# Optimization experiments

Hardware: AMD Instinct MI355X
Metric: run time of the kernel (lower is better)

## Reference

```python
import jax, jax.numpy as jnp
import numpy as np

B = 32          # number of graphs/segments
N_PER = 1024    # nodes per graph (equal segments)
N = B * N_PER
DIM = 3
SIGMA = 0.2


def setup_inputs() -> dict:
    key = jax.random.key(0)
    k1, k2, k3, k4 = jax.random.split(key, 4)
    src_pos = jax.random.normal(k1, (N, DIM), dtype=jnp.float32)
    tgt_pos = jax.random.normal(k2, (N, DIM), dtype=jnp.float32)
    # equal-sized contiguous segments: 0,0,...,1,1,...,B-1
    src_batch = jnp.repeat(jnp.arange(B, dtype=jnp.int64), N_PER)
    tgt_batch = jnp.repeat(jnp.arange(B, dtype=jnp.int64), N_PER)
    W = jax.random.normal(k3, (1, 2), dtype=jnp.float32) * 0.5
    b = jnp.zeros((1,), dtype=jnp.float32)
    return {"src_pos": src_pos, "tgt_pos": tgt_pos,
            "src_batch": src_batch, "tgt_batch": tgt_batch,
            "W": W, "b": b}


def _segment_mean(x, seg, num_segments):
    s = jax.ops.segment_sum(x, seg, num_segments=num_segments)
    cnt = jax.ops.segment_sum(jnp.ones((x.shape[0], 1), x.dtype), seg,
                              num_segments=num_segments)
    return s / cnt


def _weight_head(pos, seg, W, b):
    # SE(3)-invariant features: squared radius from per-graph centroid + bias feature
    cent = _segment_mean(pos, seg, B)                  # [B,3]
    centered = pos - cent[seg]                          # [N,3]
    r_sq = jnp.sum(centered * centered, axis=1, keepdims=True)  # [N,1]
    feat = jnp.concatenate([r_sq, jnp.ones_like(r_sq)], axis=1)  # [N,2]
    w = jax.nn.sigmoid(feat @ W.T + b).squeeze(-1)      # [N]
    return w + 1e-4


def _gauss_kernel(x, y, sigma):
    # x:[B,n,3], y:[B,m,3] -> K:[B,n,m]
    sq = (jnp.sum(x * x, -1)[:, :, None] + jnp.sum(y * y, -1)[:, None, :]
          - 2.0 * jnp.einsum('bnd,bmd->bnm', x, y))
    return jnp.exp(-sq / (2.0 * sigma * sigma))


def _kde_mmd(src_pos, tgt_pos, src_seg, tgt_seg, w_src, w_tgt, sigma):
    # center=True: subtract per-graph centroid
    src_c = src_pos - _segment_mean(src_pos, src_seg, B)[src_seg]
    tgt_c = tgt_pos - _segment_mean(tgt_pos, tgt_seg, B)[tgt_seg]
    # equal-sized segments -> block-diagonal pairwise structure via reshape
    x = src_c.reshape(B, N_PER, DIM)
    y = tgt_c.reshape(B, N_PER, DIM)
    wx = w_src.reshape(B, N_PER)
    wy = w_tgt.reshape(B, N_PER)
    # normalize weights per segment (KDE mixture weights)
    wx = wx / jnp.sum(wx, axis=1, keepdims=True)
    wy = wy / jnp.sum(wy, axis=1, keepdims=True)
    kxx = _gauss_kernel(x, x, sigma)
    kyy = _gauss_kernel(y, y, sigma)
    kxy = _gauss_kernel(x, y, sigma)
    txx = jnp.einsum('bn,bnm,bm->b', wx, kxx, wx)
    tyy = jnp.einsum('bn,bnm,bm->b', wy, kyy, wy)
    txy = jnp.einsum('bn,bnm,bm->b', wx, kxy, wy)
    per_graph = txx + tyy - 2.0 * txy                   # [B]
    return jnp.mean(per_graph)


def reference(src_pos, tgt_pos, src_batch, tgt_batch, W, b):
    w_src = _weight_head(src_pos, src_batch, W, b)
    w_tgt = _weight_head(tgt_pos, tgt_batch, W, b)
    loss = _kde_mmd(src_pos, tgt_pos, src_batch, tgt_batch, w_src, w_tgt, SIGMA)
    return loss
```

## Files before the change

kernel.cpp:

```cpp
#include <hip/hip_runtime.h>

#define BGR 32
#define N_PER 1024
#define NEGC (-18.033688011112043f)
#define SCAL (36.067376022224086f)
#define NBLK (8 * BGR * 3)

__device__ __forceinline__ float fast_exp2(float x) {
#if __has_builtin(__builtin_amdgcn_exp2f)
    return __builtin_amdgcn_exp2f(x);
#else
    return exp2f(x);
#endif
}


__global__ __launch_bounds__(256) void prep_kernel(
    const float* __restrict__ src_pos, const float* __restrict__ tgt_pos,
    const float* __restrict__ W, const float* __restrict__ bias,
    float4* __restrict__ nodebuf, float* __restrict__ wsum,
    float* __restrict__ T, int* __restrict__ counter)
{
    const int blk  = blockIdx.x;
    const int side = blk >> 5;
    const int b    = blk & 31;
    const float* pos = (side ? tgt_pos : src_pos) + (size_t)b * N_PER * 3;
    const int t = threadIdx.x;
    const int lane = t & 63, wv = t >> 6;

    const float4* p4 = (const float4*)pos;
    float4 p0 = p4[3*t + 0];
    float4 p1 = p4[3*t + 1];
    float4 p2 = p4[3*t + 2];
    float nx[4] = {p0.x, p0.w, p1.z, p2.y};
    float ny[4] = {p0.y, p1.x, p1.w, p2.z};
    float nz[4] = {p0.z, p1.y, p2.x, p2.w};

    float sx = nx[0]+nx[1]+nx[2]+nx[3];
    float sy = ny[0]+ny[1]+ny[2]+ny[3];
    float sz = nz[0]+nz[1]+nz[2]+nz[3];
    #pragma unroll
    for (int off = 32; off; off >>= 1) {
        sx += __shfl_down(sx, off);
        sy += __shfl_down(sy, off);
        sz += __shfl_down(sz, off);
    }
    __shared__ float shred[12];
    __shared__ float cent[3];
    if (lane == 0) { shred[wv*3+0] = sx; shred[wv*3+1] = sy; shred[wv*3+2] = sz; }
    __syncthreads();
    if (t == 0) {
        float cx = 0.f, cy = 0.f, cz = 0.f;
        #pragma unroll
        for (int i = 0; i < 4; i++) { cx += shred[i*3]; cy += shred[i*3+1]; cz += shred[i*3+2]; }
        cent[0] = cx * (1.f/N_PER); cent[1] = cy * (1.f/N_PER); cent[2] = cz * (1.f/N_PER);
    }
    __syncthreads();
    const float cx = cent[0], cy = cent[1], cz = cent[2];
    const float w0 = W[0], w1b = W[1] + bias[0];

    float4 outv[4];
    float lwsum = 0.f;
    #pragma unroll
    for (int i = 0; i < 4; i++) {
        float x = nx[i] - cx, y = ny[i] - cy, z = nz[i] - cz;
        float rsq = x*x + y*y + z*z;
        float logit = rsq * w0 + w1b;
        float w = 1.f / (1.f + __expf(-logit)) + 1e-4f;
        lwsum += w;
        float A = fmaf(NEGC, rsq, __log2f(w));
        outv[i] = make_float4(x, y, z, A);
    }
    float4* outp = nodebuf + ((size_t)(side*BGR + b)) * N_PER + t*4;
    outp[0] = outv[0]; outp[1] = outv[1]; outp[2] = outv[2]; outp[3] = outv[3];

    #pragma unroll
    for (int off = 32; off; off >>= 1) lwsum += __shfl_down(lwsum, off);
    __shared__ float shw[4];
    if (lane == 0) shw[wv] = lwsum;
    __syncthreads();
    if (t == 0) wsum[side*BGR + b] = shw[0] + shw[1] + shw[2] + shw[3];

    if (blk == 0) {
        if (t < 3*BGR) T[t] = 0.f;
        if (t == 0) *counter = 0;
    }
}

__global__ __launch_bounds__(256) void pair_kernel(
    const float4* __restrict__ nodebuf, const float* __restrict__ wsum,
    float* __restrict__ T, int* __restrict__ counter, float* __restrict__ out)
{
    const int tile = blockIdx.x;
    const int b    = blockIdx.y;
    const int kind = blockIdx.z;
    const int rowside = (kind == 1) ? 1 : 0;
    const int colside = (kind == 0) ? 0 : 1;
    const float4* rows = nodebuf + ((size_t)(rowside*BGR + b)) * N_PER;
    const float4* cols = nodebuf + ((size_t)(colside*BGR + b)) * N_PER;

    __shared__ float4 lds[N_PER];
    const int t = threadIdx.x;
    #pragma unroll
    for (int i = 0; i < 4; i++) lds[t + 256*i] = cols[t + 256*i];
    __syncthreads();

    const int lane = t & 63, q = t >> 6;
    const int r0 = tile*128 + lane;
    const float4 ra = rows[r0];
    const float4 rb = rows[r0 + 64];
    const float rax = SCAL*ra.x, ray = SCAL*ra.y, raz = SCAL*ra.z, raA = ra.w;
    const float rbx = SCAL*rb.x, rby = SCAL*rb.y, rbz = SCAL*rb.z, rbA = rb.w;
    float acca = 0.f, accb = 0.f;
    const int m0 = q * 256;
    #pragma unroll 8
    for (int m = m0; m < m0 + 256; ++m) {
        float4 c = lds[m];
        float ta = fmaf(rax, c.x, c.w + raA);
        ta = fmaf(ray, c.y, ta);
        ta = fmaf(raz, c.z, ta);
        acca += fast_exp2(ta);
        float tb = fmaf(rbx, c.x, c.w + rbA);
        tb = fmaf(rby, c.y, tb);
        tb = fmaf(rbz, c.z, tb);
        accb += fast_exp2(tb);
    }
    float acc = acca + accb;
    #pragma unroll
    for (int off = 32; off; off >>= 1) acc += __shfl_down(acc, off);
    __shared__ float sh[4];
    __shared__ int islast;
    if (lane == 0) sh[q] = acc;
    __syncthreads();
    if (t == 0) {
        atomicAdd(&T[kind*BGR + b], sh[0] + sh[1] + sh[2] + sh[3]);
        __threadfence();
        int old = __hip_atomic_fetch_add(counter, 1, __ATOMIC_ACQ_REL,
                                         __HIP_MEMORY_SCOPE_AGENT);
        islast = (old == NBLK - 1);
    }
    __syncthreads();
    if (islast) {
        float v = 0.f;
        if (t < BGR) {
            float Sx = wsum[t], Sy = wsum[BGR + t];
            float txx = __hip_atomic_load(&T[t],        __ATOMIC_RELAXED, __HIP_MEMORY_SCOPE_AGENT);
            float tyy = __hip_atomic_load(&T[BGR + t],  __ATOMIC_RELAXED, __HIP_MEMORY_SCOPE_AGENT);
            float txy = __hip_atomic_load(&T[2*BGR + t],__ATOMIC_RELAXED, __HIP_MEMORY_SCOPE_AGENT);
            v = txx / (Sx * Sx) + tyy / (Sy * Sy) - 2.f * txy / (Sx * Sy);
        }
        if (t < 64) {
            #pragma unroll
            for (int off = 32; off; off >>= 1) v += __shfl_down(v, off);
            if (t == 0) out[0] = v * (1.f / BGR);
        }
    }
}

extern "C" void kernel_launch(void* const* d_in, const int* in_sizes, int n_in,
                              void* d_out, int out_size, void* d_ws, size_t ws_size,
                              hipStream_t stream) {
    const float* src_pos = (const float*)d_in[0];
    const float* tgt_pos = (const float*)d_in[1];
    const float* W    = (const float*)d_in[4];
    const float* bias = (const float*)d_in[5];

    float4* nodebuf = (float4*)d_ws;
    float*  wsum    = (float*)((char*)d_ws + (size_t)2 * BGR * N_PER * sizeof(float4));
    float*  T       = (float*)((char*)d_ws + (size_t)2 * BGR * N_PER * sizeof(float4) + 256);
    int*    counter = (int*)  ((char*)d_ws + (size_t)2 * BGR * N_PER * sizeof(float4) + 1024);

    prep_kernel<<<64, 256, 0, stream>>>(src_pos, tgt_pos, W, bias,
                                        nodebuf, wsum, T, counter);
    pair_kernel<<<dim3(8, BGR, 3), 256, 0, stream>>>(nodebuf, wsum, T, counter,
                                                     (float*)d_out);
}
```

Baseline: 99.28 us.

## Fuse node preprocessing into pair kernel and replace atomics with partial-sum combine

Each pair block now recomputes the centroid, weights and log-weight terms for its column segment, and for the cross term also its 128 source rows, directly into LDS. This removes the separate prep kernel and the global node buffer round trip. The atomic accumulation and last-block counter are replaced by per-tile partial sums plus a tiny combine kernel. The cost is redundant preprocessing: each segment is rebuilt by every tile, and cross-term blocks do a second build pass.

Measured after the change: 84.88 us. -14.5%, faster.

```diff
diff --git a/kernel.cpp b/kernel.cpp
--- a/kernel.cpp
+++ b/kernel.cpp
@@ -4,7 +4,6 @@
 #define N_PER 1024
 #define NEGC (-18.033688011112043f)
 #define SCAL (36.067376022224086f)
-#define NBLK (8 * BGR * 3)
 
 __device__ __forceinline__ float fast_exp2(float x) {
 #if __has_builtin(__builtin_amdgcn_exp2f)
@@ -15,19 +14,12 @@
 }
 
 
-__global__ __launch_bounds__(256) void prep_kernel(
-    const float* __restrict__ src_pos, const float* __restrict__ tgt_pos,
-    const float* __restrict__ W, const float* __restrict__ bias,
-    float4* __restrict__ nodebuf, float* __restrict__ wsum,
-    float* __restrict__ T, int* __restrict__ counter)
+__device__ __forceinline__ void build_side(
+    const float* __restrict__ pos, int t, int lane, int wv,
+    float w0, float w1b, float4* __restrict__ dest, int mode, int rowbase,
+    float* __restrict__ shred, float* __restrict__ cent, float* __restrict__ shw,
+    bool do_wsum, float* __restrict__ wsum_out)
 {
-    const int blk  = blockIdx.x;
-    const int side = blk >> 5;
-    const int b    = blk & 31;
-    const float* pos = (side ? tgt_pos : src_pos) + (size_t)b * N_PER * 3;
-    const int t = threadIdx.x;
-    const int lane = t & 63, wv = t >> 6;
-
     const float4* p4 = (const float4*)pos;
     float4 p0 = p4[3*t + 0];
     float4 p1 = p4[3*t + 1];
@@ -45,8 +37,6 @@
         sy += __shfl_down(sy, off);
         sz += __shfl_down(sz, off);
     }
-    __shared__ float shred[12];
-    __shared__ float cent[3];
     if (lane == 0) { shred[wv*3+0] = sx; shred[wv*3+1] = sy; shred[wv*3+2] = sz; }
     __syncthreads();
     if (t == 0) {
@@ -57,9 +47,7 @@
     }
     __syncthreads();
     const float cx = cent[0], cy = cent[1], cz = cent[2];
-    const float w0 = W[0], w1b = W[1] + bias[0];
 
-    float4 outv[4];
     float lwsum = 0.f;
     #pragma unroll
     for (int i = 0; i < 4; i++) {
@@ -69,53 +57,64 @@
         float w = 1.f / (1.f + __expf(-logit)) + 1e-4f;
         lwsum += w;
         float A = fmaf(NEGC, rsq, __log2f(w));
-        outv[i] = make_float4(x, y, z, A);
+        float4 v = make_float4(x, y, z, A);
+        int gi = 4*t + i;
+        if (mode == 0) {
+            dest[gi] = v;
+        } else {
+            unsigned ri = (unsigned)(gi - rowbase);
+            if (ri < 128u) dest[ri] = v;
+        }
     }
-    float4* outp = nodebuf + ((size_t)(side*BGR + b)) * N_PER + t*4;
-    outp[0] = outv[0]; outp[1] = outv[1]; outp[2] = outv[2]; outp[3] = outv[3];
-
     #pragma unroll
     for (int off = 32; off; off >>= 1) lwsum += __shfl_down(lwsum, off);
-    __shared__ float shw[4];
     if (lane == 0) shw[wv] = lwsum;
     __syncthreads();
-    if (t == 0) wsum[side*BGR + b] = shw[0] + shw[1] + shw[2] + shw[3];
-
-    if (blk == 0) {
-        if (t < 3*BGR) T[t] = 0.f;
-        if (t == 0) *counter = 0;
-    }
+    if (do_wsum && t == 0) wsum_out[0] = shw[0] + shw[1] + shw[2] + shw[3];
 }
 
-__global__ __launch_bounds__(256) void pair_kernel(
-    const float4* __restrict__ nodebuf, const float* __restrict__ wsum,
-    float* __restrict__ T, int* __restrict__ counter, float* __restrict__ out)
+__global__ __launch_bounds__(256) void fused_kernel(
+    const float* __restrict__ src_pos, const float* __restrict__ tgt_pos,
+    const float* __restrict__ W, const float* __restrict__ bias,
+    float* __restrict__ Tpart, float* __restrict__ wsum)
 {
     const int tile = blockIdx.x;
     const int b    = blockIdx.y;
     const int kind = blockIdx.z;
-    const int rowside = (kind == 1) ? 1 : 0;
-    const int colside = (kind == 0) ? 0 : 1;
-    const float4* rows = nodebuf + ((size_t)(rowside*BGR + b)) * N_PER;
-    const float4* cols = nodebuf + ((size_t)(colside*BGR + b)) * N_PER;
+    const int t = threadIdx.x;
+    const int lane = t & 63, wv = t >> 6;
 
-    __shared__ float4 lds[N_PER];
-    const int t = threadIdx.x;
-    #pragma unroll
-    for (int i = 0; i < 4; i++) lds[t + 256*i] = cols[t + 256*i];
+    __shared__ float4 ldsc[N_PER];
+    __shared__ float4 ldsr[128];
+    __shared__ float shred[12];
+    __shared__ float cent[3];
+    __shared__ float shw[4];
+
+    const float w0 = W[0], w1b = W[1] + bias[0];
+    const float* srcb = src_pos + (size_t)b * N_PER * 3;
+    const float* tgtb = tgt_pos + (size_t)b * N_PER * 3;
+
+    const float* colpos = (kind == 0) ? srcb : tgtb;
+    build_side(colpos, t, lane, wv, w0, w1b, ldsc, 0, 0,
+               shred, cent, shw, kind < 2, &wsum[kind*BGR + b]);
+
+    if (kind == 2) {
+        build_side(srcb, t, lane, wv, w0, w1b, ldsr, 1, tile*128,
+                   shred, cent, shw, false, nullptr);
+    }
     __syncthreads();
 
-    const int lane = t & 63, q = t >> 6;
+    const int q = t >> 6;
     const int r0 = tile*128 + lane;
-    const float4 ra = rows[r0];
-    const float4 rb = rows[r0 + 64];
+    const float4 ra = (kind == 2) ? ldsr[lane]      : ldsc[r0];
+    const float4 rb = (kind == 2) ? ldsr[lane + 64] : ldsc[r0 + 64];
     const float rax = SCAL*ra.x, ray = SCAL*ra.y, raz = SCAL*ra.z, raA = ra.w;
     const float rbx = SCAL*rb.x, rby = SCAL*rb.y, rbz = SCAL*rb.z, rbA = rb.w;
     float acca = 0.f, accb = 0.f;
     const int m0 = q * 256;
     #pragma unroll 8
     for (int m = m0; m < m0 + 256; ++m) {
-        float4 c = lds[m];
+        float4 c = ldsc[m];
         float ta = fmaf(rax, c.x, c.w + raA);
         ta = fmaf(ray, c.y, ta);
         ta = fmaf(raz, c.z, ta);
@@ -128,33 +127,32 @@
     float acc = acca + accb;
     #pragma unroll
     for (int off = 32; off; off >>= 1) acc += __shfl_down(acc, off);
-    __shared__ float sh[4];
-    __shared__ int islast;
-    if (lane == 0) sh[q] = acc;
+    if (lane == 0) shw[q] = acc;
     __syncthreads();
-    if (t == 0) {
-        atomicAdd(&T[kind*BGR + b], sh[0] + sh[1] + sh[2] + sh[3]);
-        __threadfence();
-        int old = __hip_atomic_fetch_add(counter, 1, __ATOMIC_ACQ_REL,
-                                         __HIP_MEMORY_SCOPE_AGENT);
-        islast = (old == NBLK - 1);
+    if (t == 0) Tpart[(kind*BGR + b)*8 + tile] = shw[0] + shw[1] + shw[2] + shw[3];
+}
+
+__global__ __launch_bounds__(64) void combine_kernel(
+    const float* __restrict__ Tpart, const float* __restrict__ wsum,
+    float* __restrict__ out)
+{
+    const int t = threadIdx.x;
+    float v = 0.f;
+    if (t < BGR) {
+        float Sx = wsum[t], Sy = wsum[BGR + t];
+        float s[3];
+        #pragma unroll
+        for (int k = 0; k < 3; k++) {
+            float acc = 0.f;
+            #pragma unroll
+            for (int j = 0; j < 8; j++) acc += Tpart[(k*BGR + t)*8 + j];
+            s[k] = acc;
+        }
+        v = s[0] / (Sx * Sx) + s[1] / (Sy * Sy) - 2.f * s[2] / (Sx * Sy);
     }
-    __syncthreads();
-    if (islast) {
-        float v = 0.f;
-        if (t < BGR) {
-            float Sx = wsum[t], Sy = wsum[BGR + t];
-            float txx = __hip_atomic_load(&T[t],        __ATOMIC_RELAXED, __HIP_MEMORY_SCOPE_AGENT);
-            float tyy = __hip_atomic_load(&T[BGR + t],  __ATOMIC_RELAXED, __HIP_MEMORY_SCOPE_AGENT);
-            float txy = __hip_atomic_load(&T[2*BGR + t],__ATOMIC_RELAXED, __HIP_MEMORY_SCOPE_AGENT);
-            v = txx / (Sx * Sx) + tyy / (Sy * Sy) - 2.f * txy / (Sx * Sy);
-        }
-        if (t < 64) {
-            #pragma unroll
-            for (int off = 32; off; off >>= 1) v += __shfl_down(v, off);
-            if (t == 0) out[0] = v * (1.f / BGR);
-        }
-    }
+    #pragma unroll
+    for (int off = 32; off; off >>= 1) v += __shfl_down(v, off);
+    if (t == 0) out[0] = v * (1.f / BGR);
 }
 
 extern "C" void kernel_launch(void* const* d_in, const int* in_sizes, int n_in,
@@ -165,13 +163,10 @@
     const float* W    = (const float*)d_in[4];
     const float* bias = (const float*)d_in[5];
 
-    float4* nodebuf = (float4*)d_ws;
-    float*  wsum    = (float*)((char*)d_ws + (size_t)2 * BGR * N_PER * sizeof(float4));
-    float*  T       = (float*)((char*)d_ws + (size_t)2 * BGR * N_PER * sizeof(float4) + 256);
-    int*    counter = (int*)  ((char*)d_ws + (size_t)2 * BGR * N_PER * sizeof(float4) + 1024);
+    float* Tpart = (float*)d_ws;
+    float* wsum  = (float*)d_ws + 3*BGR*8;
 
-    prep_kernel<<<64, 256, 0, stream>>>(src_pos, tgt_pos, W, bias,
-                                        nodebuf, wsum, T, counter);
-    pair_kernel<<<dim3(8, BGR, 3), 256, 0, stream>>>(nodebuf, wsum, T, counter,
-                                                     (float*)d_out);
+    fused_kernel<<<dim3(8, BGR, 3), 256, 0, stream>>>(src_pos, tgt_pos, W, bias,
+                                                      Tpart, wsum);
+    combine_kernel<<<1, 64, 0, stream>>>(Tpart, wsum, (float*)d_out);
 }
```
